# Performance work log

Hardware: AMD Instinct MI355X
Metric: run time of the kernel (lower is better)

Reference implementation:

```python
import jax, jax.numpy as jnp
import numpy as np

B, T, EMB, HID, NCLS = 256, 512, 128, 256, 32000


def _forward(X, C_table, U_i, V_i, b_i, U_f, V_f, b_f, U_c, V_c, b_c, U_o, V_o, b_o,
             U_i1, V_i1, b_i1, U_f1, V_f1, b_f1, U_c1, V_c1, b_c1, U_o1, V_o1, b_o1,
             W_w, b_out):
    E = C_table[X]  # [B, T, EMB]
    # Layer 0: in the source, h_t0 and c_t0 are NEVER reassigned inside the loop,
    # so they remain zeros for every timestep. Hence h_t0 @ V_* == 0 and
    # f_t * c_t0 == 0, and layer 0 is time-independent -> vectorize over T.
    i0 = jax.nn.sigmoid(jnp.einsum('bte,eh->bth', E, U_i) + b_i)
    g0 = jnp.tanh(jnp.einsum('bte,eh->bth', E, U_c) + b_c)
    o0 = jax.nn.sigmoid(jnp.einsum('bte,eh->bth', E, U_o) + b_o)
    c0 = i0 * g0               # f_t * c_t0 term is exactly zero
    h0 = o0 * jnp.tanh(c0)     # [B, T, HID]

    # Layer 1: true recurrence over its own (h_t1, c_t1) state, fed by layer-0 h.
    # Computed for faithfulness; the source's output ignores it (results holds h_t).
    def step(carry, x):
        h1, c1 = carry
        i1 = jax.nn.sigmoid(x @ U_i1 + h1 @ V_i1 + b_i1)
        g1 = jnp.tanh(x @ U_c1 + h1 @ V_c1 + b_c1)
        f1 = jax.nn.sigmoid(x @ U_f1 + h1 @ V_f1 + b_f1)
        o1 = jax.nn.sigmoid(x @ U_o1 + h1 @ V_o1 + b_o1)
        c1n = f1 * c1 + i1 * g1
        h1n = o1 * jnp.tanh(c1n)
        return (h1n, c1n), None

    zeros = jnp.zeros((h0.shape[0], HID), dtype=h0.dtype)
    _carry, _ = jax.lax.scan(step, (zeros, zeros), jnp.swapaxes(h0, 0, 1))

    # outputs = results[-1] = layer-0 hidden at the last timestep
    logits = h0[:, -1, :] @ W_w.T + b_out  # [B, NCLS]
    return logits


def setup_inputs() -> dict:
    key = jax.random.key(0)
    ks = jax.random.split(key, 32)

    def p(k, *shape):
        return (jax.random.normal(k, shape, dtype=jnp.float32) * 0.02)

    inp = {
        'X': jax.random.randint(ks[0], (B, T), 0, NCLS, dtype=jnp.int32),
        'C_table': p(ks[1], NCLS, EMB),
        'U_i': p(ks[2], EMB, HID), 'V_i': p(ks[3], HID, HID), 'b_i': p(ks[4], HID),
        'U_f': p(ks[5], EMB, HID), 'V_f': p(ks[6], HID, HID), 'b_f': p(ks[7], HID),
        'U_c': p(ks[8], EMB, HID), 'V_c': p(ks[9], HID, HID), 'b_c': p(ks[10], HID),
        'U_o': p(ks[11], EMB, HID), 'V_o': p(ks[12], HID, HID), 'b_o': p(ks[13], HID),
        'U_i1': p(ks[14], HID, HID), 'V_i1': p(ks[15], HID, HID), 'b_i1': p(ks[16], HID),
        'U_f1': p(ks[17], HID, HID), 'V_f1': p(ks[18], HID, HID), 'b_f1': p(ks[19], HID),
        'U_c1': p(ks[20], HID, HID), 'V_c1': p(ks[21], HID, HID), 'b_c1': p(ks[22], HID),
        'U_o1': p(ks[23], HID, HID), 'V_o1': p(ks[24], HID, HID), 'b_o1': p(ks[25], HID),
        'W_w': p(ks[26], NCLS, HID),
        'b_out': jnp.ones((NCLS,), dtype=jnp.float32),
    }
    return inp


def reference(X, C_table, U_i, V_i, b_i, U_f, V_f, b_f, U_c, V_c, b_c, U_o, V_o, b_o,
              U_i1, V_i1, b_i1, U_f1, V_f1, b_f1, U_c1, V_c1, b_c1, U_o1, V_o1, b_o1,
              W_w, b_out):
    return _forward(X, C_table, U_i, V_i, b_i, U_f, V_f, b_f, U_c, V_c, b_c,
                    U_o, V_o, b_o, U_i1, V_i1, b_i1, U_f1, V_f1, b_f1,
                    U_c1, V_c1, b_c1, U_o1, V_o1, b_o1, W_w, b_out)
```

## Files before the change

### kernel.cpp

```cpp
#include <hip/hip_runtime.h>

#define B_SZ   256
#define T_SZ   512
#define EMB    128
#define HID    256
#define NCLS   32000

typedef __attribute__((ext_vector_type(8))) short short8;
typedef __attribute__((ext_vector_type(4))) float f32x4;

__device__ inline unsigned short bf16rne(float f) {
    union { float f; unsigned int u; } v; v.f = f;
    unsigned int u = v.u;
    u += 0x7FFFu + ((u >> 16) & 1u);
    return (unsigned short)(u >> 16);
}

__device__ inline unsigned pkhi(float lo, float hi) {
    union { float f; unsigned u; } a, b;
    a.f = lo; b.f = hi;
    return ((b.u + 0x8000u) & 0xFFFF0000u) | ((a.u + 0x8000u) >> 16);
}


__global__ __launch_bounds__(256)
void lstm_h_last(const int* __restrict__ X, const float* __restrict__ C_table,
                 const float* __restrict__ U_i, const float* __restrict__ b_i,
                 const float* __restrict__ U_c, const float* __restrict__ b_c,
                 const float* __restrict__ U_o, const float* __restrict__ b_o,
                 unsigned short* __restrict__ hws) {
    __shared__ float e[EMB];
    const int m = blockIdx.x;
    const int k = threadIdx.x;

    const int token = X[(size_t)m * T_SZ + (T_SZ - 1)];
    if (k < EMB) e[k] = C_table[(size_t)token * EMB + k];
    __syncthreads();

    float ai = 0.f, ac = 0.f, ao = 0.f;
    #pragma unroll
    for (int c = 0; c < 4; ++c) {
        float ui[32], uc[32], uo[32];
        #pragma unroll
        for (int j = 0; j < 32; ++j) {
            const int ee = c * 32 + j;
            ui[j] = U_i[ee * HID + k];
            uc[j] = U_c[ee * HID + k];
            uo[j] = U_o[ee * HID + k];
        }
        #pragma unroll
        for (int j = 0; j < 32; ++j)
            asm volatile("" : "+v"(ui[j]), "+v"(uc[j]), "+v"(uo[j]));
        #pragma unroll
        for (int j = 0; j < 32; ++j) {
            const float ev = e[c * 32 + j];
            ai += ev * ui[j]; ac += ev * uc[j]; ao += ev * uo[j];
        }
    }

    const float i0 = 1.f / (1.f + expf(-(ai + b_i[k])));
    const float g0 = tanhf(ac + b_c[k]);
    const float o0 = 1.f / (1.f + expf(-(ao + b_o[k])));
    const unsigned short hv = bf16rne(o0 * tanhf(i0 * g0));

    const int frag_id = (m >> 4) * 8 + (k >> 5);
    const int lane_in = ((k >> 3) & 3) * 16 + (m & 15);
    hws[frag_id * 512 + lane_in * 8 + (k & 7)] = hv;
}

__global__ __launch_bounds__(512, 2)
void logits_gemm(const unsigned short* __restrict__ hws,
                 const float* __restrict__ Ww,
                 const float* __restrict__ b_out,
                 float* __restrict__ out) {
    __shared__ unsigned short Hs[B_SZ * HID];

    const int t    = threadIdx.x;
    const int wid  = t >> 6;
    const int lane = t & 63;
    const int l15  = lane & 15;
    const int lq   = lane >> 4;

    const int nbase = blockIdx.x * 128 + wid * 16;

    const float* wrow = Ww + (size_t)(nbase + l15) * HID + lq * 8;
    f32x4 wf[16];
    #pragma unroll
    for (int ks = 0; ks < 8; ++ks) {
        wf[2 * ks]     = *reinterpret_cast<const f32x4*>(wrow + ks * 32);
        wf[2 * ks + 1] = *reinterpret_cast<const f32x4*>(wrow + ks * 32 + 4);
    }

    #pragma unroll
    for (int j = 0; j < 16; ++j) {
        const unsigned short* src = hws + (wid * 16 + j) * 512;
        __builtin_amdgcn_global_load_lds(
            (const __attribute__((address_space(1))) unsigned int*)(src + lane * 8),
            (__attribute__((address_space(3))) unsigned int*)(Hs + (wid * 16 + j) * 512),
            16, 0, 0);
    }

    #pragma unroll
    for (int i = 0; i < 16; ++i) asm volatile("" : "+v"(wf[i]));
    asm volatile("s_waitcnt vmcnt(0)" ::: "memory");
    __builtin_amdgcn_s_barrier();
    __builtin_amdgcn_sched_barrier(0);

    short8 aw[8];
    #pragma unroll
    for (int ks = 0; ks < 8; ++ks) {
        union { short8 s; unsigned u[4]; } p;
        p.u[0] = pkhi(wf[2 * ks][0],     wf[2 * ks][1]);
        p.u[1] = pkhi(wf[2 * ks][2],     wf[2 * ks][3]);
        p.u[2] = pkhi(wf[2 * ks + 1][0], wf[2 * ks + 1][1]);
        p.u[3] = pkhi(wf[2 * ks + 1][2], wf[2 * ks + 1][3]);
        aw[ks] = p.s;
    }

    f32x4 bv = *reinterpret_cast<const f32x4*>(b_out + nbase + lq * 4);

    const unsigned short* hbase = Hs + lane * 8;
    f32x4 acc[16] = {};
    #pragma unroll
    for (int ks = 0; ks < 8; ++ks) {
        #pragma unroll
        for (int mf = 0; mf < 16; ++mf) {
            short8 bh = *reinterpret_cast<const short8*>(
                hbase + (mf * 8 + ks) * 512);
            acc[mf] = __builtin_amdgcn_mfma_f32_16x16x32_bf16(
                aw[ks], bh, acc[mf], 0, 0, 0);
        }
    }

    #pragma unroll
    for (int mf = 0; mf < 16; ++mf) {
        f32x4 o = acc[mf] + bv;
        *reinterpret_cast<f32x4*>(
            out + (size_t)(mf * 16 + l15) * NCLS + nbase + lq * 4) = o;
    }
}

extern "C" void kernel_launch(void* const* d_in, const int* in_sizes, int n_in,
                              void* d_out, int out_size, void* d_ws, size_t ws_size,
                              hipStream_t stream) {
    const int*   X       = (const int*)  d_in[0];
    const float* C_table = (const float*)d_in[1];
    const float* U_i     = (const float*)d_in[2];
    const float* b_i     = (const float*)d_in[4];
    const float* U_c     = (const float*)d_in[8];
    const float* b_c     = (const float*)d_in[10];
    const float* U_o     = (const float*)d_in[11];
    const float* b_o     = (const float*)d_in[13];
    const float* W_w     = (const float*)d_in[26];
    const float* b_out   = (const float*)d_in[27];
    float* out = (float*)d_out;

    unsigned short* hws = (unsigned short*)d_ws;

    lstm_h_last<<<B_SZ, 256, 0, stream>>>(X, C_table, U_i, b_i, U_c, b_c,
                                          U_o, b_o, hws);
    logits_gemm<<<NCLS / 128, 512, 0, stream>>>(hws, W_w, b_out, out);
}
```

Baseline: 30.14 us.

## Split embedding reduction across waves and process two batch rows per block

Restructures the h_last kernel so each block handles two batch rows with 512 threads. The embedding dimension is split across 8 waves, each using float4 loads of the U matrices, and partial sums are reduced through shared memory. This is meant to shorten each thread's serial dependency chain, vectorize the weight loads and reuse each weight load across two rows. In exchange it adds a shared-memory reduction, an extra barrier, and output packing that now uses round-half-up pkhi instead of the round-to-nearest-even bf16rne.

```diff
diff --git a/kernel.cpp b/kernel.cpp
--- a/kernel.cpp
+++ b/kernel.cpp
@@ -15,7 +15,6 @@
     u += 0x7FFFu + ((u >> 16) & 1u);
     return (unsigned short)(u >> 16);
 }
-
 __device__ inline unsigned pkhi(float lo, float hi) {
     union { float f; unsigned u; } a, b;
     a.f = lo; b.f = hi;
@@ -23,49 +22,78 @@
 }
 
 
-__global__ __launch_bounds__(256)
+__global__ __launch_bounds__(512, 2)
 void lstm_h_last(const int* __restrict__ X, const float* __restrict__ C_table,
                  const float* __restrict__ U_i, const float* __restrict__ b_i,
                  const float* __restrict__ U_c, const float* __restrict__ b_c,
                  const float* __restrict__ U_o, const float* __restrict__ b_o,
                  unsigned short* __restrict__ hws) {
-    __shared__ float e[EMB];
-    const int m = blockIdx.x;
-    const int k = threadIdx.x;
+    __shared__ float e[2][EMB];
+    __shared__ int   tok[2];
+    __shared__ f32x4 part[8][3][2][64];
 
-    const int token = X[(size_t)m * T_SZ + (T_SZ - 1)];
-    if (k < EMB) e[k] = C_table[(size_t)token * EMB + k];
+    const int t    = threadIdx.x;
+    const int wid  = t >> 6;
+    const int lane = t & 63;
+    const int m0   = blockIdx.x * 2;
+    const int kb   = lane * 4;
+
+    if (t < 2) tok[t] = X[(size_t)(m0 + t) * T_SZ + (T_SZ - 1)];
+    __syncthreads();
+    if (t < 256) e[t >> 7][t & 127] =
+        C_table[(size_t)tok[t >> 7] * EMB + (t & 127)];
     __syncthreads();
 
-    float ai = 0.f, ac = 0.f, ao = 0.f;
-    #pragma unroll
-    for (int c = 0; c < 4; ++c) {
-        float ui[32], uc[32], uo[32];
+    f32x4 acc[3][2] = {};
+    #pragma unroll 4
+    for (int j = 0; j < 16; ++j) {
+        const int ee = wid * 16 + j;
+        const f32x4 ui = *reinterpret_cast<const f32x4*>(U_i + (size_t)ee * HID + kb);
+        const f32x4 uc = *reinterpret_cast<const f32x4*>(U_c + (size_t)ee * HID + kb);
+        const f32x4 uo = *reinterpret_cast<const f32x4*>(U_o + (size_t)ee * HID + kb);
         #pragma unroll
-        for (int j = 0; j < 32; ++j) {
-            const int ee = c * 32 + j;
-            ui[j] = U_i[ee * HID + k];
-            uc[j] = U_c[ee * HID + k];
-            uo[j] = U_o[ee * HID + k];
-        }
-        #pragma unroll
-        for (int j = 0; j < 32; ++j)
-            asm volatile("" : "+v"(ui[j]), "+v"(uc[j]), "+v"(uo[j]));
-        #pragma unroll
-        for (int j = 0; j < 32; ++j) {
-            const float ev = e[c * 32 + j];
-            ai += ev * ui[j]; ac += ev * uc[j]; ao += ev * uo[j];
+        for (int r = 0; r < 2; ++r) {
+            const float ev = e[r][ee];
+            acc[0][r] += ev * ui;
+            acc[1][r] += ev * uc;
+            acc[2][r] += ev * uo;
         }
     }
+    #pragma unroll
+    for (int g = 0; g < 3; ++g)
+        #pragma unroll
+        for (int r = 0; r < 2; ++r)
+            part[wid][g][r][lane] = acc[g][r];
+    __syncthreads();
 
-    const float i0 = 1.f / (1.f + expf(-(ai + b_i[k])));
-    const float g0 = tanhf(ac + b_c[k]);
-    const float o0 = 1.f / (1.f + expf(-(ao + b_o[k])));
-    const unsigned short hv = bf16rne(o0 * tanhf(i0 * g0));
-
-    const int frag_id = (m >> 4) * 8 + (k >> 5);
-    const int lane_in = ((k >> 3) & 3) * 16 + (m & 15);
-    hws[frag_id * 512 + lane_in * 8 + (k & 7)] = hv;
+    if (t < 128) {
+        const int r = wid;
+        const int m = m0 + r;
+        f32x4 s[3];
+        #pragma unroll
+        for (int g = 0; g < 3; ++g) {
+            s[g] = part[0][g][r][lane];
+            #pragma unroll
+            for (int w = 1; w < 8; ++w) s[g] += part[w][g][r][lane];
+        }
+        const f32x4 bi = *reinterpret_cast<const f32x4*>(b_i + kb);
+        const f32x4 bc = *reinterpret_cast<const f32x4*>(b_c + kb);
+        const f32x4 bo = *reinterpret_cast<const f32x4*>(b_o + kb);
+        float h[4];
+        #pragma unroll
+        for (int c = 0; c < 4; ++c) {
+            const float i0 = 1.f / (1.f + expf(-(s[0][c] + bi[c])));
+            const float g0 = tanhf(s[1][c] + bc[c]);
+            const float o0 = 1.f / (1.f + expf(-(s[2][c] + bo[c])));
+            h[c] = o0 * tanhf(i0 * g0);
+        }
+        const int frag = (m >> 4) * 8 + (lane >> 3);
+        const int li   = ((lane >> 1) & 3) * 16 + (m & 15);
+        unsigned* dst = reinterpret_cast<unsigned*>(
+            hws + frag * 512 + li * 8 + (lane & 1) * 4);
+        dst[0] = pkhi(h[0], h[1]);
+        dst[1] = pkhi(h[2], h[3]);
+    }
 }
 
 __global__ __launch_bounds__(512, 2)
@@ -157,7 +185,7 @@
 
     unsigned short* hws = (unsigned short*)d_ws;
 
-    lstm_h_last<<<B_SZ, 256, 0, stream>>>(X, C_table, U_i, b_i, U_c, b_c,
-                                          U_o, b_o, hws);
+    lstm_h_last<<<B_SZ / 2, 512, 0, stream>>>(X, C_table, U_i, b_i, U_c, b_c,
+                                              U_o, b_o, hws);
     logits_gemm<<<NCLS / 128, 512, 0, stream>>>(hws, W_w, b_out, out);
 }
```

After: 28.54 us. 5.3% less time.
